# Kernel optimization log

Measured on AMD Instinct MI355X. Metric: run time of the kernel, lower is better.

The kernel has to match this reference:

```python
import jax, jax.numpy as jnp
import numpy as np

BLOCK_SIZE = 64


def _dequant_weight(weight_packed, centroids, scales):
    # weight_packed: [out, in//2] bytes; each byte packs two 4-bit codes.
    # torch.cartesian_prod ordering: byte v -> (centroids[v >> 4], centroids[v & 0xF])
    hi = weight_packed >> 4
    lo = weight_packed & 0xF
    out_f, packed_in = weight_packed.shape
    w = jnp.stack([centroids[hi], centroids[lo]], axis=-1).reshape(out_f, packed_in * 2)
    num_blocks = scales.shape[1]
    w = (w.reshape(out_f, num_blocks, -1) * scales[:, :, None]).reshape(out_f, packed_in * 2)
    return w  # [out, in]


def setup_inputs() -> dict:
    key = jax.random.key(0)
    k1, k2, k3, k4 = jax.random.split(key, 4)
    B, S, IN, OUT = 2, 4096, 4096, 4096
    x = jax.random.normal(k1, (B, S, IN), dtype=jnp.float32)
    weight_packed = jax.random.randint(k2, (OUT, IN // 2), 0, 256, dtype=jnp.int32)
    centroids = jax.random.normal(k3, (16,), dtype=jnp.float32)
    scales = jax.random.uniform(k4, (OUT, IN // BLOCK_SIZE), dtype=jnp.float32)
    return {"x": x, "weight_packed": weight_packed, "centroids": centroids, "scales": scales}


def reference(x, weight_packed, centroids, scales):
    orig_shape = x.shape
    in_features = orig_shape[-1]
    x_flat = x.reshape(-1, in_features)  # [M, in]
    w = _dequant_weight(weight_packed, centroids, scales)  # [out, in]
    out = x_flat @ w.T  # [M, out]
    return out.reshape(*orig_shape[:-1], w.shape[0])
```

## Files before the change

kernel.cpp:

```cpp
#include <hip/hip_runtime.h>
#include <hip/hip_bf16.h>
#include <stdint.h>

typedef __bf16 bf16_t;
typedef bf16_t bf16x4 __attribute__((ext_vector_type(4)));
typedef bf16_t bf16x8 __attribute__((ext_vector_type(8)));
typedef float f32x4 __attribute__((ext_vector_type(4)));

#define GAS __attribute__((address_space(1)))
#define LAS __attribute__((address_space(3)))

__device__ __forceinline__ void async_load16(const void* g, void* l) {
    __builtin_amdgcn_global_load_lds((const GAS void*)g, (LAS void*)l, 16, 0, 0);
}

__device__ __forceinline__ void hw_barrier() {
    asm volatile("" ::: "memory");
    __builtin_amdgcn_s_barrier();
    asm volatile("" ::: "memory");
}

__global__ __launch_bounds__(256) void prep_kernel(
    const float* __restrict__ x, bf16_t* __restrict__ xb,
    const int* __restrict__ wp, const float* __restrict__ cen,
    const float* __restrict__ scl, bf16_t* __restrict__ W,
    int castBlocks, long nCastChunks, int nDeqChunks)
{
    if ((int)blockIdx.x < castBlocks) {
        long idx    = (long)blockIdx.x * blockDim.x + threadIdx.x;
        long stride = (long)castBlocks * blockDim.x;
        const float4* xv = (const float4*)x;
        bf16x8* xo = (bf16x8*)xb;
        for (long t = idx; t < nCastChunks; t += stride) {
            float4 a = xv[2 * t];
            float4 b = xv[2 * t + 1];
            bf16x8 o;
            o[0] = (bf16_t)a.x; o[1] = (bf16_t)a.y; o[2] = (bf16_t)a.z; o[3] = (bf16_t)a.w;
            o[4] = (bf16_t)b.x; o[5] = (bf16_t)b.y; o[6] = (bf16_t)b.z; o[7] = (bf16_t)b.w;
            xo[t] = o;
        }
    } else {
        __shared__ float c[16];
        if (threadIdx.x < 16) c[threadIdx.x] = cen[threadIdx.x];
        __syncthreads();
        int  nb     = (int)gridDim.x - castBlocks;
        long idx    = (long)((int)blockIdx.x - castBlocks) * blockDim.x + threadIdx.x;
        long stride = (long)nb * blockDim.x;
        const int4* wv = (const int4*)wp;
        bf16x8* wo = (bf16x8*)W;
        for (long t = idx; t < (long)nDeqChunks; t += stride) {
            int4 v = wv[t];
            long p   = t << 2;
            int  o   = (int)(p >> 11);
            int  pin = (int)p & 2047;
            float s = scl[(o << 6) + (pin >> 5)];
            int vv[4] = {v.x, v.y, v.z, v.w};
            bf16x8 outv;
#pragma unroll
            for (int i = 0; i < 4; ++i) {
                int b = vv[i];
                outv[2 * i]     = (bf16_t)(c[(b >> 4) & 15] * s);
                outv[2 * i + 1] = (bf16_t)(c[b & 15] * s);
            }
            wo[t] = outv;
        }
    }
}

#define BM 256
#define BN 256
#define BK 64

__global__ __launch_bounds__(512, 2) void gemm_bf16_nt(
    const bf16_t* __restrict__ A, const bf16_t* __restrict__ B,
    float* __restrict__ C, int M, int N, int K)
{
    __shared__ bf16_t lA[2][BM * BK];
    __shared__ bf16_t lB[2][BN * BK];

    const int tid  = threadIdx.x;
    const int wave = tid >> 6;
    const int lane = tid & 63;
    const int wmB  = (wave >> 2) * 128;
    const int wnB  = (wave & 3) * 64;

    const int nwg = (int)gridDim.x;
    const int cpx = nwg >> 3;
    const int bid = (int)blockIdx.x;
    const int swz = (bid & 7) * cpx + (bid >> 3);
    const int nx  = N / BN;
    const int by  = swz / nx;
    const int bx  = swz - by * nx;
    const long m0 = (long)by * BM;
    const long n0 = (long)bx * BN;

    int offA[4], offB[4], ldsOff[4];
#pragma unroll
    for (int r = 0; r < 4; ++r) {
        int s   = r * 512 + tid;
        int row = s >> 3;
        int kg  = (s & 7) ^ (row & 7);
        offA[r] = (int)(m0 + row) * K + kg * 8;
        offB[r] = (int)(n0 + row) * K + kg * 8;
        ldsOff[r] = (r * 512 + wave * 64) * 8;
    }

    auto stage = [&](int buf, int k0) {
#pragma unroll
        for (int r = 0; r < 4; ++r) async_load16(A + offA[r] + k0, &lA[buf][ldsOff[r]]);
#pragma unroll
        for (int r = 0; r < 4; ++r) async_load16(B + offB[r] + k0, &lB[buf][ldsOff[r]]);
    };

    const int qm  = lane & 15;
    const int kcb = lane >> 4;
    const int co0 = (kcb ^ (qm & 7)) * 8;
    const int co1 = ((kcb + 4) ^ (qm & 7)) * 8;

    f32x4 acc[8][4] = {};

    stage(0, 0);
    stage(1, BK);
    asm volatile("s_waitcnt vmcnt(8)" ::: "memory");
    hw_barrier();

    const int NT = K / BK;
    for (int j = 0; j < NT; ++j) {
        const int c = j & 1;
        const bf16_t* la = &lA[c][0];
        const bf16_t* lb = &lB[c][0];

        bf16x8 bfv[4][2], af[4][2];
#pragma unroll
        for (int nf = 0; nf < 4; ++nf) {
            const bf16_t* pb = lb + (wnB + nf * 16 + qm) * BK;
            bfv[nf][0] = *(const bf16x8*)(pb + co0);
            bfv[nf][1] = *(const bf16x8*)(pb + co1);
        }
#pragma unroll
        for (int mf = 0; mf < 4; ++mf) {
            const bf16_t* pa = la + (wmB + mf * 16 + qm) * BK;
            af[mf][0] = *(const bf16x8*)(pa + co0);
            af[mf][1] = *(const bf16x8*)(pa + co1);
        }
        __builtin_amdgcn_s_setprio(1);
#pragma unroll
        for (int mf = 0; mf < 4; ++mf)
#pragma unroll
            for (int nf = 0; nf < 4; ++nf) {
                acc[mf][nf] = __builtin_amdgcn_mfma_f32_16x16x32_bf16(af[mf][0], bfv[nf][0], acc[mf][nf], 0, 0, 0);
                acc[mf][nf] = __builtin_amdgcn_mfma_f32_16x16x32_bf16(af[mf][1], bfv[nf][1], acc[mf][nf], 0, 0, 0);
            }
        __builtin_amdgcn_s_setprio(0);
#pragma unroll
        for (int mf = 0; mf < 4; ++mf) {
            const bf16_t* pa = la + (wmB + (mf + 4) * 16 + qm) * BK;
            af[mf][0] = *(const bf16x8*)(pa + co0);
            af[mf][1] = *(const bf16x8*)(pa + co1);
        }
        __builtin_amdgcn_s_setprio(1);
#pragma unroll
        for (int mf = 0; mf < 4; ++mf)
#pragma unroll
            for (int nf = 0; nf < 4; ++nf) {
                acc[mf + 4][nf] = __builtin_amdgcn_mfma_f32_16x16x32_bf16(af[mf][0], bfv[nf][0], acc[mf + 4][nf], 0, 0, 0);
                acc[mf + 4][nf] = __builtin_amdgcn_mfma_f32_16x16x32_bf16(af[mf][1], bfv[nf][1], acc[mf + 4][nf], 0, 0, 0);
            }
        __builtin_amdgcn_s_setprio(0);

        hw_barrier();
        if (j + 2 < NT) {
            stage(c, (j + 2) * BK);
            asm volatile("s_waitcnt vmcnt(8)" ::: "memory");
        } else if (j + 1 < NT) {
            asm volatile("s_waitcnt vmcnt(0)" ::: "memory");
        }
        hw_barrier();
    }

    const int crow = (lane >> 4) * 4;
    const int ccol = lane & 15;
#pragma unroll
    for (int mf = 0; mf < 8; ++mf)
#pragma unroll
        for (int r = 0; r < 4; ++r) {
            float* cp = C + (m0 + wmB + mf * 16 + crow + r) * (long)N + (n0 + wnB + ccol);
#pragma unroll
            for (int nf = 0; nf < 4; ++nf)
                cp[nf * 16] = acc[mf][nf][r];
        }
}

__global__ void fallback_qgemm(const float* __restrict__ x, const int* __restrict__ wp,
                               const float* __restrict__ cen, const float* __restrict__ scl,
                               float* __restrict__ out, int M, int N, int Kp) {
    __shared__ float c[16];
    if (threadIdx.x < 16) c[threadIdx.x] = cen[threadIdx.x];
    __syncthreads();
    int n = blockIdx.x * blockDim.x + threadIdx.x;
    int m = blockIdx.y;
    if (n >= N) return;
    const float* xr = x + (long)m * (Kp * 2);
    const int*   wr = wp + (long)n * Kp;
    int nb = Kp / 32;
    float acc = 0.f;
    for (int b = 0; b < nb; ++b) {
        float s  = scl[n * nb + b];
        float pa = 0.f;
        for (int j = 0; j < 32; ++j) {
            int v = wr[b * 32 + j];
            pa += xr[(b * 32 + j) * 2]     * c[(v >> 4) & 15]
                + xr[(b * 32 + j) * 2 + 1] * c[v & 15];
        }
        acc += s * pa;
    }
    out[(long)m * N + n] = acc;
}

extern "C" void kernel_launch(void* const* d_in, const int* in_sizes, int n_in,
                              void* d_out, int out_size, void* d_ws, size_t ws_size,
                              hipStream_t stream) {
    const float* x   = (const float*)d_in[0];
    const int*   wp  = (const int*)d_in[1];
    const float* cen = (const float*)d_in[2];
    const float* scl = (const float*)d_in[3];
    float* out = (float*)d_out;

    const int  IN  = 4096;
    const int  OUT = 4096;
    const long M   = (long)in_sizes[0] / IN;

    size_t need = (size_t)(M * IN + (long)OUT * IN) * sizeof(bf16_t);
    if (ws_size >= need && (M % BM) == 0) {
        bf16_t* xb = (bf16_t*)d_ws;
        bf16_t* Wb = xb + M * IN;
        const int castBlocks = 2048;
        const int deqBlocks  = 512;
        long nCastChunks = M * IN / 8;
        int  nDeqChunks  = OUT * (IN / 2) / 4;
        prep_kernel<<<dim3(castBlocks + deqBlocks), dim3(256), 0, stream>>>(
            x, xb, wp, cen, scl, Wb, castBlocks, nCastChunks, nDeqChunks);
        int nwg = (OUT / BN) * (int)(M / BM);
        gemm_bf16_nt<<<dim3(nwg), dim3(512), 0, stream>>>(xb, Wb, out, (int)M, OUT, IN);
    } else {
        dim3 grid(OUT / 256, (unsigned)M);
        fallback_qgemm<<<grid, dim3(256), 0, stream>>>(x, wp, cen, scl, out, (int)M, OUT, IN / 2);
    }
}
```

Measured before the change: 520.0 us.

## Shrink GEMM tile to 256x128 with triple-buffered LDS and split staging

Changes the GEMM tile from 256x256 to 256x128 and moves to a 4x2 wave layout with a 64x64 sub-tile per wave. LDS goes from double to triple buffering, and the global-to-LDS prefetch for tile t+2 is split into two halves interleaved with the two MFMA phases. Extra barriers and explicit lgkmcnt waits are added around each phase. The aim is better overlap of loads with MFMA work and more workgroups to spread across CUs, at the cost of lower arithmetic intensity per tile, occupancy reduced to 1 block per CU, and more barriers per iteration.

```diff
diff --git a/kernel.cpp b/kernel.cpp
--- a/kernel.cpp
+++ b/kernel.cpp
@@ -3,7 +3,6 @@
 #include <stdint.h>
 
 typedef __bf16 bf16_t;
-typedef bf16_t bf16x4 __attribute__((ext_vector_type(4)));
 typedef bf16_t bf16x8 __attribute__((ext_vector_type(8)));
 typedef float f32x4 __attribute__((ext_vector_type(4)));
 
@@ -13,7 +12,6 @@
 __device__ __forceinline__ void async_load16(const void* g, void* l) {
     __builtin_amdgcn_global_load_lds((const GAS void*)g, (LAS void*)l, 16, 0, 0);
 }
-
 __device__ __forceinline__ void hw_barrier() {
     asm volatile("" ::: "memory");
     __builtin_amdgcn_s_barrier();
@@ -68,21 +66,22 @@
 }
 
 #define BM 256
-#define BN 256
+#define BN 128
 #define BK 64
-
-__global__ __launch_bounds__(512, 2) void gemm_bf16_nt(
+#define NBUF 3
+
+__global__ __launch_bounds__(512, 1) void gemm_bf16_nt(
     const bf16_t* __restrict__ A, const bf16_t* __restrict__ B,
     float* __restrict__ C, int M, int N, int K)
 {
-    __shared__ bf16_t lA[2][BM * BK];
-    __shared__ bf16_t lB[2][BN * BK];
+    __shared__ bf16_t lA[NBUF * BM * BK];
+    __shared__ bf16_t lB[NBUF * BN * BK];
 
     const int tid  = threadIdx.x;
     const int wave = tid >> 6;
     const int lane = tid & 63;
-    const int wmB  = (wave >> 2) * 128;
-    const int wnB  = (wave & 3) * 64;
+    const int wm4  = (wave >> 1) * 64;
+    const int wn2  = (wave & 1) * 64;
 
     const int nwg = (int)gridDim.x;
     const int cpx = nwg >> 3;
@@ -94,100 +93,126 @@
     const long m0 = (long)by * BM;
     const long n0 = (long)bx * BN;
 
-    int offA[4], offB[4], ldsOff[4];
+    int offA[4], offB[2], ldsA[4], ldsB[2];
 #pragma unroll
     for (int r = 0; r < 4; ++r) {
-        int s   = r * 512 + tid;
+        int s = r * 512 + tid;
         int row = s >> 3;
-        int kg  = (s & 7) ^ (row & 7);
+        int kg = (s & 7) ^ (row & 7);
         offA[r] = (int)(m0 + row) * K + kg * 8;
+        ldsA[r] = (r * 512 + wave * 64) * 8;
+    }
+#pragma unroll
+    for (int r = 0; r < 2; ++r) {
+        int s = r * 512 + tid;
+        int row = s >> 3;
+        int kg = (s & 7) ^ (row & 7);
         offB[r] = (int)(n0 + row) * K + kg * 8;
-        ldsOff[r] = (r * 512 + wave * 64) * 8;
-    }
-
-    auto stage = [&](int buf, int k0) {
-#pragma unroll
-        for (int r = 0; r < 4; ++r) async_load16(A + offA[r] + k0, &lA[buf][ldsOff[r]]);
-#pragma unroll
-        for (int r = 0; r < 4; ++r) async_load16(B + offB[r] + k0, &lB[buf][ldsOff[r]]);
-    };
+        ldsB[r] = (r * 512 + wave * 64) * 8;
+    }
 
     const int qm  = lane & 15;
     const int kcb = lane >> 4;
     const int co0 = (kcb ^ (qm & 7)) * 8;
     const int co1 = ((kcb + 4) ^ (qm & 7)) * 8;
 
-    f32x4 acc[8][4] = {};
-
-    stage(0, 0);
-    stage(1, BK);
-    asm volatile("s_waitcnt vmcnt(8)" ::: "memory");
+    f32x4 acc[4][4] = {};
+
+#pragma unroll
+    for (int r = 0; r < 4; ++r) async_load16(A + offA[r], lA + ldsA[r]);
+#pragma unroll
+    for (int r = 0; r < 2; ++r) async_load16(B + offB[r], lB + ldsB[r]);
+#pragma unroll
+    for (int r = 0; r < 4; ++r) async_load16(A + offA[r] + BK, lA + BM * BK + ldsA[r]);
+#pragma unroll
+    for (int r = 0; r < 2; ++r) async_load16(B + offB[r] + BK, lB + BN * BK + ldsB[r]);
+    asm volatile("s_waitcnt vmcnt(6)" ::: "memory");
     hw_barrier();
 
     const int NT = K / BK;
-    for (int j = 0; j < NT; ++j) {
-        const int c = j & 1;
-        const bf16_t* la = &lA[c][0];
-        const bf16_t* lb = &lB[c][0];
-
-        bf16x8 bfv[4][2], af[4][2];
-#pragma unroll
-        for (int nf = 0; nf < 4; ++nf) {
-            const bf16_t* pb = lb + (wnB + nf * 16 + qm) * BK;
-            bfv[nf][0] = *(const bf16x8*)(pb + co0);
-            bfv[nf][1] = *(const bf16x8*)(pb + co1);
-        }
-#pragma unroll
-        for (int mf = 0; mf < 4; ++mf) {
-            const bf16_t* pa = la + (wmB + mf * 16 + qm) * BK;
-            af[mf][0] = *(const bf16x8*)(pa + co0);
-            af[mf][1] = *(const bf16x8*)(pa + co1);
-        }
+    int cb = 0, sb = 2;
+    for (int t = 0; t < NT; ++t) {
+        const bf16_t* la = lA + cb * (BM * BK);
+        const bf16_t* lb = lB + cb * (BN * BK);
+        bf16_t* sa = lA + sb * (BM * BK);
+        bf16_t* sv = lB + sb * (BN * BK);
+        const int  kt2     = (t + 2) * BK;
+        const bool doStage = (t + 2 < NT);
+
+        bf16x8 bfr[4][2], af[2][2];
+
+        if (doStage) {
+            async_load16(A + offA[0] + kt2, sa + ldsA[0]);
+            async_load16(A + offA[1] + kt2, sa + ldsA[1]);
+            async_load16(B + offB[0] + kt2, sv + ldsB[0]);
+        }
+#pragma unroll
+        for (int j = 0; j < 4; ++j) {
+            const bf16_t* pb = lb + (wn2 + j * 16 + qm) * BK;
+            bfr[j][0] = *(const bf16x8*)(pb + co0);
+            bfr[j][1] = *(const bf16x8*)(pb + co1);
+        }
+#pragma unroll
+        for (int i = 0; i < 2; ++i) {
+            const bf16_t* pa = la + (wm4 + i * 16 + qm) * BK;
+            af[i][0] = *(const bf16x8*)(pa + co0);
+            af[i][1] = *(const bf16x8*)(pa + co1);
+        }
+        hw_barrier();
+        asm volatile("s_waitcnt lgkmcnt(0)" ::: "memory");
+        __builtin_amdgcn_sched_barrier(0);
         __builtin_amdgcn_s_setprio(1);
 #pragma unroll
-        for (int mf = 0; mf < 4; ++mf)
-#pragma unroll
-            for (int nf = 0; nf < 4; ++nf) {
-                acc[mf][nf] = __builtin_amdgcn_mfma_f32_16x16x32_bf16(af[mf][0], bfv[nf][0], acc[mf][nf], 0, 0, 0);
-                acc[mf][nf] = __builtin_amdgcn_mfma_f32_16x16x32_bf16(af[mf][1], bfv[nf][1], acc[mf][nf], 0, 0, 0);
+        for (int i = 0; i < 2; ++i)
+#pragma unroll
+            for (int j = 0; j < 4; ++j) {
+                acc[i][j] = __builtin_amdgcn_mfma_f32_16x16x32_bf16(af[i][0], bfr[j][0], acc[i][j], 0, 0, 0);
+                acc[i][j] = __builtin_amdgcn_mfma_f32_16x16x32_bf16(af[i][1], bfr[j][1], acc[i][j], 0, 0, 0);
             }
         __builtin_amdgcn_s_setprio(0);
-#pragma unroll
-        for (int mf = 0; mf < 4; ++mf) {
-            const bf16_t* pa = la + (wmB + (mf + 4) * 16 + qm) * BK;
-            af[mf][0] = *(const bf16x8*)(pa + co0);
-            af[mf][1] = *(const bf16x8*)(pa + co1);
-        }
+        hw_barrier();
+
+        if (doStage) {
+            async_load16(A + offA[2] + kt2, sa + ldsA[2]);
+            async_load16(A + offA[3] + kt2, sa + ldsA[3]);
+            async_load16(B + offB[1] + kt2, sv + ldsB[1]);
+        }
+#pragma unroll
+        for (int i = 0; i < 2; ++i) {
+            const bf16_t* pa = la + (wm4 + (i + 2) * 16 + qm) * BK;
+            af[i][0] = *(const bf16x8*)(pa + co0);
+            af[i][1] = *(const bf16x8*)(pa + co1);
+        }
+        hw_barrier();
+        asm volatile("s_waitcnt lgkmcnt(0)" ::: "memory");
+        __builtin_amdgcn_sched_barrier(0);
         __builtin_amdgcn_s_setprio(1);
 #pragma unroll
-        for (int mf = 0; mf < 4; ++mf)
-#pragma unroll
-            for (int nf = 0; nf < 4; ++nf) {
-                acc[mf + 4][nf] = __builtin_amdgcn_mfma_f32_16x16x32_bf16(af[mf][0], bfv[nf][0], acc[mf + 4][nf], 0, 0, 0);
-                acc[mf + 4][nf] = __builtin_amdgcn_mfma_f32_16x16x32_bf16(af[mf][1], bfv[nf][1], acc[mf + 4][nf], 0, 0, 0);
+        for (int i = 0; i < 2; ++i)
+#pragma unroll
+            for (int j = 0; j < 4; ++j) {
+                acc[i + 2][j] = __builtin_amdgcn_mfma_f32_16x16x32_bf16(af[i][0], bfr[j][0], acc[i + 2][j], 0, 0, 0);
+                acc[i + 2][j] = __builtin_amdgcn_mfma_f32_16x16x32_bf16(af[i][1], bfr[j][1], acc[i + 2][j], 0, 0, 0);
             }
         __builtin_amdgcn_s_setprio(0);
-
-        hw_barrier();
-        if (j + 2 < NT) {
-            stage(c, (j + 2) * BK);
-            asm volatile("s_waitcnt vmcnt(8)" ::: "memory");
-        } else if (j + 1 < NT) {
-            asm volatile("s_waitcnt vmcnt(0)" ::: "memory");
-        }
-        hw_barrier();
+        if (doStage)              asm volatile("s_waitcnt vmcnt(6)" ::: "memory");
+        else if (t + 1 < NT)      asm volatile("s_waitcnt vmcnt(0)" ::: "memory");
+        hw_barrier();
+
+        cb = (cb == NBUF - 1) ? 0 : cb + 1;
+        sb = (sb == NBUF - 1) ? 0 : sb + 1;
     }
 
     const int crow = (lane >> 4) * 4;
     const int ccol = lane & 15;
 #pragma unroll
-    for (int mf = 0; mf < 8; ++mf)
+    for (int i = 0; i < 4; ++i)
 #pragma unroll
         for (int r = 0; r < 4; ++r) {
-            float* cp = C + (m0 + wmB + mf * 16 + crow + r) * (long)N + (n0 + wnB + ccol);
-#pragma unroll
-            for (int nf = 0; nf < 4; ++nf)
-                cp[nf * 16] = acc[mf][nf][r];
+            float* cp = C + (m0 + wm4 + i * 16 + crow + r) * (long)N + (n0 + wn2 + ccol);
+#pragma unroll
+            for (int j = 0; j < 4; ++j)
+                cp[j * 16] = acc[i][j][r];
         }
 }
 
```

Measured after the change: 753.2 us. 44.8% more time.
